# Performance work log

Measured on AMD Instinct MI355X. Metric: run time of the kernel, lower is better.

The kernel has to match this reference:

```python
import jax, jax.numpy as jnp
import numpy as np

H = 1024
S = 8192
B = 1  # module's broadcast in the weighted-sum step only supports B == 1


def setup_inputs() -> dict:
    key = jax.random.key(0)
    k1, k2, k3 = jax.random.split(key, 3)
    scale = 1.0 / np.sqrt(H)
    enc_out = jax.random.normal(k1, (B, S, H), dtype=jnp.float32)
    w1 = jax.random.normal(k2, (H, H), dtype=jnp.float32) * scale  # nn.Linear weight [out,in]
    w2 = jax.random.normal(k3, (H, H), dtype=jnp.float32) * scale
    return {"enc_out": enc_out, "w1": w1, "w2": w2}


def reference(enc_out, w1, w2):
    # attn_weights = tanh(w1(enc_out)) @ w2(enc_out)^T  -> [B, S, S]
    q = jnp.tanh(jnp.einsum('bsh,oh->bso', enc_out, w1))
    k = jnp.einsum('bsh,oh->bso', enc_out, w2)
    scores = jnp.einsum('bih,bjh->bij', q, k)          # [B, S, S]
    attn = jax.nn.softmax(scores, axis=1)               # softmax over dim=1 (rows)
    # torch: sum over dim=1 of attn[B,S,S,1] * enc_out broadcast as [1,B,S,H].
    # For B==1 this equals enc_out[0,j,h] * sum_i attn[0,i,j]; avoid the
    # [B,S,S,H] intermediate the eager torch code materializes.
    col_sum = jnp.sum(attn, axis=1)                     # [B, S]
    context = col_sum[..., None] * enc_out              # [B, S, H]
    return context, attn
```

## Files before the change

### kernel.cpp

```cpp
#include <hip/hip_runtime.h>
#include <hip/hip_bf16.h>
#include <math.h>


typedef _Float16 half_t;
typedef _Float16 half8 __attribute__((ext_vector_type(8)));
typedef _Float16 half4 __attribute__((ext_vector_type(4)));
typedef float f32x4 __attribute__((ext_vector_type(4)));

#define S_DIM 8192
#define H_DIM 1024

__device__ __forceinline__ void gload16(const void* g, void* l) {
  __builtin_amdgcn_global_load_lds(
      (const __attribute__((address_space(1))) void*)g,
      (__attribute__((address_space(3))) void*)l, 16, 0, 0);
}

__global__ void __launch_bounds__(256) k_cvt(const float* __restrict__ src,
                                             half_t* __restrict__ dst) {
  long g = (long)blockIdx.x * 256 + threadIdx.x;
  f32x4 x = ((const f32x4*)src)[g];
  half4 h;
#pragma unroll
  for (int e = 0; e < 4; ++e) h[e] = (half_t)x[e];
  ((half4*)dst)[g] = h;
}

#define GEMM_MAINLOOP(APTR, BPTR)                                              \
  __shared__ half_t As[8192];                                                  \
  __shared__ half_t Bs[8192];                                                  \
  const int tid = threadIdx.x;                                                 \
  const int lane = tid & 63;                                                   \
  const int quad = lane >> 4;                                                  \
  const int l15 = lane & 15;                                                   \
  const int wave = tid >> 6;                                                   \
  const int wm = wave & 1;                                                     \
  const int wn = wave >> 1;                                                    \
  int aoff[4], boff[4], loff[4];                                               \
  _Pragma("unroll") for (int t = 0; t < 4; ++t) {                              \
    int f8 = t * 256 + tid;                                                    \
    int u = f8 >> 7;                                                           \
    int m = f8 & 127;                                                          \
    aoff[t] = (bm * 128 + m) * H_DIM + u * 8;                                  \
    boff[t] = (bn * 128 + m) * H_DIM + u * 8;                                  \
    loff[t] = f8 * 8;                                                          \
  }                                                                            \
  f32x4 acc[4][4];                                                             \
  _Pragma("unroll") for (int r = 0; r < 4; ++r)                                \
      _Pragma("unroll") for (int c = 0; c < 4; ++c)                            \
          acc[r][c] = (f32x4){0.f, 0.f, 0.f, 0.f};                             \
  for (int k0 = 0; k0 < H_DIM; k0 += 64) {                                     \
    _Pragma("unroll") for (int t = 0; t < 4; ++t)                              \
        gload16(APTR + aoff[t] + k0, &As[loff[t]]);                            \
    _Pragma("unroll") for (int t = 0; t < 4; ++t)                              \
        gload16(BPTR + boff[t] + k0, &Bs[loff[t]]);                            \
    __syncthreads();                                                           \
    _Pragma("unroll") for (int ki = 0; ki < 2; ++ki) {                         \
      const int u = ki * 4 + quad;                                             \
      half8 af[4], bf[4];                                                      \
      _Pragma("unroll") for (int r = 0; r < 4; ++r)                            \
          af[r] = *(const half8*)&As[(u * 128 + wm * 64 + r * 16 + l15) * 8];  \
      _Pragma("unroll") for (int c = 0; c < 4; ++c)                            \
          bf[c] = *(const half8*)&Bs[(u * 128 + wn * 64 + c * 16 + l15) * 8];  \
      _Pragma("unroll") for (int r = 0; r < 4; ++r)                            \
          _Pragma("unroll") for (int c = 0; c < 4; ++c)                        \
              acc[r][c] = __builtin_amdgcn_mfma_f32_16x16x32_f16(              \
                  af[r], bf[c], acc[r][c], 0, 0, 0);                           \
    }                                                                          \
    __syncthreads();                                                           \
  }

__global__ void __launch_bounds__(256) k_gemm_qk(const half_t* __restrict__ A,
                                                 const half_t* __restrict__ B,
                                                 half_t* __restrict__ Qh,
                                                 half_t* __restrict__ Kh) {
  const int bm = blockIdx.y;
  const int bn = blockIdx.x;
  GEMM_MAINLOOP(A, B)
  const int colbase = bn * 128 + wn * 64;
  const int rowb = bm * 128 + wm * 64;
#pragma unroll
  for (int r = 0; r < 4; ++r) {
#pragma unroll
    for (int c = 0; c < 4; ++c) {
      int col = colbase + c * 16 + l15;
      int row = rowb + r * 16 + quad * 4;
#pragma unroll
      for (int v = 0; v < 4; ++v) {
        float x = acc[r][c][v];
        if (col < 1024) {
          Qh[(long)(row + v) * 1024 + col] = (half_t)tanhf(x);
        } else {
          Kh[(long)(row + v) * 1024 + (col - 1024)] = (half_t)x;
        }
      }
    }
  }
}

template <bool FUSE_STATS>
__global__ void __launch_bounds__(256) k_gemm_scores(const half_t* __restrict__ A,
                                                     const half_t* __restrict__ B,
                                                     float* __restrict__ out,
                                                     float* __restrict__ Pm,
                                                     float* __restrict__ Ps) {
  const int lin = blockIdx.x;
  const int patch = lin >> 6;
  const int local = lin & 63;
  const int bm = (patch >> 3) * 8 + (local >> 3);
  const int bn = (patch & 7) * 8 + (local & 7);
  GEMM_MAINLOOP(A, B)
  const int colbase = bn * 128 + wn * 64;
  const int rowb = bm * 128 + wm * 64;
#pragma unroll
  for (int r = 0; r < 4; ++r) {
#pragma unroll
    for (int c = 0; c < 4; ++c) {
      int col = colbase + c * 16 + l15;
      int row = rowb + r * 16 + quad * 4;
#pragma unroll
      for (int v = 0; v < 4; ++v) {
        out[(long)(row + v) * S_DIM + col] = acc[r][c][v];
      }
    }
  }
  if (FUSE_STATS) {
    float cmax[4], csum[4];
#pragma unroll
    for (int c = 0; c < 4; ++c) {
      float m = acc[0][c][0];
#pragma unroll
      for (int r = 0; r < 4; ++r)
#pragma unroll
        for (int v = 0; v < 4; ++v) m = fmaxf(m, acc[r][c][v]);
      m = fmaxf(m, __shfl_xor(m, 16, 64));
      m = fmaxf(m, __shfl_xor(m, 32, 64));
      cmax[c] = m;
      float s = 0.f;
#pragma unroll
      for (int r = 0; r < 4; ++r)
#pragma unroll
        for (int v = 0; v < 4; ++v) s += __expf(acc[r][c][v] - m);
      s += __shfl_xor(s, 16, 64);
      s += __shfl_xor(s, 32, 64);
      csum[c] = s;
    }
    float* sred = (float*)As;
    if (quad == 0) {
#pragma unroll
      for (int c = 0; c < 4; ++c) {
        int idx = ((((wm * 2 + wn) * 4 + c) * 16 + l15) * 2);
        sred[idx] = cmax[c];
        sred[idx + 1] = csum[c];
      }
    }
    __syncthreads();
    if (wm == 0 && quad == 0) {
#pragma unroll
      for (int c = 0; c < 4; ++c) {
        int i0 = ((((0 * 2 + wn) * 4 + c) * 16 + l15) * 2);
        int i1 = ((((1 * 2 + wn) * 4 + c) * 16 + l15) * 2);
        float m0 = sred[i0], s0 = sred[i0 + 1];
        float m1 = sred[i1], s1 = sred[i1 + 1];
        float M = fmaxf(m0, m1);
        float Ssum = s0 * __expf(m0 - M) + s1 * __expf(m1 - M);
        int col = colbase + c * 16 + l15;
        Pm[(long)bm * S_DIM + col] = M;
        Ps[(long)bm * S_DIM + col] = Ssum;
      }
    }
  }
}

__global__ void __launch_bounds__(256) k_colstats(const float* __restrict__ P,
                                                  float* __restrict__ Pm,
                                                  float* __restrict__ Ps) {
  const int c = threadIdx.x & 63;
  const int rg = threadIdx.x >> 6;
  const int j = blockIdx.x * 64 + c;
  const int seg = blockIdx.y;
  float m = -3.0e38f, s = 0.f;
  for (int t = 0; t < 256; ++t) {
    int i = seg * 1024 + t * 4 + rg;
    float x = P[(long)i * S_DIM + j];
    float mn = fmaxf(m, x);
    s = s * __expf(m - mn) + __expf(x - mn);
    m = mn;
  }
  __shared__ float sm[4][64];
  __shared__ float ss[4][64];
  sm[rg][c] = m;
  ss[rg][c] = s;
  __syncthreads();
  if (threadIdx.x < 64) {
    float mm = sm[0][c];
#pragma unroll
    for (int r = 1; r < 4; ++r) mm = fmaxf(mm, sm[r][c]);
    float sum = 0.f;
#pragma unroll
    for (int r = 0; r < 4; ++r) sum += ss[r][c] * __expf(sm[r][c] - mm);
    Pm[seg * S_DIM + j] = mm;
    Ps[seg * S_DIM + j] = sum;
  }
}

__global__ void __launch_bounds__(256) k_combine(const float* __restrict__ Pm,
                                                 const float* __restrict__ Ps,
                                                 float* __restrict__ Mcol,
                                                 float* __restrict__ Rcol,
                                                 int nseg) {
  int j = blockIdx.x * 256 + threadIdx.x;
  float m = Pm[j];
  for (int r = 1; r < nseg; ++r) m = fmaxf(m, Pm[(long)r * S_DIM + j]);
  float s = 0.f;
  for (int r = 0; r < nseg; ++r)
    s += Ps[(long)r * S_DIM + j] * __expf(Pm[(long)r * S_DIM + j] - m);
  Mcol[j] = m;
  Rcol[j] = 1.0f / s;
}

__global__ void __launch_bounds__(256) k_norm(float* __restrict__ P,
                                              const float* __restrict__ Mcol,
                                              const float* __restrict__ Rcol,
                                              const f32x4* __restrict__ enc,
                                              f32x4* __restrict__ ctx) {
  long b = blockIdx.x;
  if (b >= 65536) {
    long g = (b - 65536) * 256 + threadIdx.x;
    ctx[g] = enc[g];
    return;
  }
  long gid = b * 256 + threadIdx.x;
  int j4 = (int)(gid & 2047);
  f32x4 x = ((const f32x4*)P)[gid];
  f32x4 a = ((const f32x4*)Mcol)[j4];
  f32x4 r = ((const f32x4*)Rcol)[j4];
  f32x4 o;
#pragma unroll
  for (int e = 0; e < 4; ++e) o[e] = __expf(x[e] - a[e]) * r[e];
  ((f32x4*)P)[gid] = o;
}

extern "C" void kernel_launch(void* const* d_in, const int* in_sizes, int n_in,
                              void* d_out, int out_size, void* d_ws, size_t ws_size,
                              hipStream_t stream) {
  const float* enc = (const float*)d_in[0];
  const float* w1 = (const float*)d_in[1];
  const float* w2 = (const float*)d_in[2];

  float* out = (float*)d_out;
  float* ctx = out;
  float* attn = out + 8388608;

  half_t* Qh = (half_t*)ctx;
  half_t* Kh = Qh + 8388608;
  half_t* enc_h = (half_t*)attn;
  half_t* w_h = (half_t*)((char*)attn + 16777216);

  const bool fuse = ws_size >= (size_t)(64 + 64 + 2) * S_DIM * 4;
  const int nseg = fuse ? 64 : 8;
  char* ws = (char*)d_ws;
  float* Pm = (float*)ws;
  float* Ps = (float*)(ws + (size_t)nseg * S_DIM * 4);
  float* Mcol = (float*)(ws + (size_t)2 * nseg * S_DIM * 4);
  float* Rcol = Mcol + S_DIM;

  k_cvt<<<8192, 256, 0, stream>>>(enc, enc_h);
  k_cvt<<<1024, 256, 0, stream>>>(w1, w_h);
  k_cvt<<<1024, 256, 0, stream>>>(w2, w_h + 1048576);

  k_gemm_qk<<<dim3(16, 64), 256, 0, stream>>>(enc_h, w_h, Qh, Kh);

  if (fuse) {
    k_gemm_scores<true><<<4096, 256, 0, stream>>>(Qh, Kh, attn, Pm, Ps);
  } else {
    k_gemm_scores<false><<<4096, 256, 0, stream>>>(Qh, Kh, attn, Pm, Ps);
    k_colstats<<<dim3(128, 8), 256, 0, stream>>>(attn, Pm, Ps);
  }
  k_combine<<<32, 256, 0, stream>>>(Pm, Ps, Mcol, Rcol, nseg);

  k_norm<<<73728, 256, 0, stream>>>(attn, Mcol, Rcol, (const f32x4*)enc,
                                    (f32x4*)ctx);
}
```

Measured before the change: 766.8 us.

## Use 256x256 GEMM tiles with a 4-stage async LDS pipeline

```diff
diff --git a/kernel.cpp b/kernel.cpp
--- a/kernel.cpp
+++ b/kernel.cpp
@@ -16,6 +16,8 @@
       (const __attribute__((address_space(1))) void*)g,
       (__attribute__((address_space(3))) void*)l, 16, 0, 0);
 }
+
+#define WAITVM(N) asm volatile("s_waitcnt vmcnt(" #N ")" ::: "memory")
 
 __global__ void __launch_bounds__(256) k_cvt(const float* __restrict__ src,
                                              half_t* __restrict__ dst) {
@@ -27,97 +29,112 @@
   ((half4*)dst)[g] = h;
 }
 
-#define GEMM_MAINLOOP(APTR, BPTR)                                              \
-  __shared__ half_t As[8192];                                                  \
-  __shared__ half_t Bs[8192];                                                  \
+#define GEMM_MAINLOOP_256(APTR, BPTR)                                          \
+  __shared__ __align__(16) half_t As[4][8192];                                 \
+  __shared__ __align__(16) half_t Bs[4][8192];                                 \
   const int tid = threadIdx.x;                                                 \
   const int lane = tid & 63;                                                   \
   const int quad = lane >> 4;                                                  \
   const int l15 = lane & 15;                                                   \
   const int wave = tid >> 6;                                                   \
-  const int wm = wave & 1;                                                     \
-  const int wn = wave >> 1;                                                    \
-  int aoff[4], boff[4], loff[4];                                               \
-  _Pragma("unroll") for (int t = 0; t < 4; ++t) {                              \
-    int f8 = t * 256 + tid;                                                    \
-    int u = f8 >> 7;                                                           \
-    int m = f8 & 127;                                                          \
-    aoff[t] = (bm * 128 + m) * H_DIM + u * 8;                                  \
-    boff[t] = (bn * 128 + m) * H_DIM + u * 8;                                  \
+  const int wm = wave >> 2;                                          \
+  const int wn = wave & 3;                                           \
+  int aoff[2], boff[2], loff[2];                                               \
+  _Pragma("unroll") for (int t = 0; t < 2; ++t) {                              \
+    int f8 = t * 512 + tid;                                       \
+    int u = f8 >> 8;                                                 \
+    int m = f8 & 255;                                                          \
+    aoff[t] = (bm * 256 + m) * H_DIM + u * 8;                                  \
+    boff[t] = (bn * 256 + m) * H_DIM + u * 8;                                  \
     loff[t] = f8 * 8;                                                          \
   }                                                                            \
-  f32x4 acc[4][4];                                                             \
-  _Pragma("unroll") for (int r = 0; r < 4; ++r)                                \
+  f32x4 acc[8][4];                                                             \
+  _Pragma("unroll") for (int r = 0; r < 8; ++r)                                \
       _Pragma("unroll") for (int c = 0; c < 4; ++c)                            \
           acc[r][c] = (f32x4){0.f, 0.f, 0.f, 0.f};                             \
-  for (int k0 = 0; k0 < H_DIM; k0 += 64) {                                     \
-    _Pragma("unroll") for (int t = 0; t < 4; ++t)                              \
-        gload16(APTR + aoff[t] + k0, &As[loff[t]]);                            \
-    _Pragma("unroll") for (int t = 0; t < 4; ++t)                              \
-        gload16(BPTR + boff[t] + k0, &Bs[loff[t]]);                            \
-    __syncthreads();                                                           \
-    _Pragma("unroll") for (int ki = 0; ki < 2; ++ki) {                         \
-      const int u = ki * 4 + quad;                                             \
-      half8 af[4], bf[4];                                                      \
-      _Pragma("unroll") for (int r = 0; r < 4; ++r)                            \
-          af[r] = *(const half8*)&As[(u * 128 + wm * 64 + r * 16 + l15) * 8];  \
-      _Pragma("unroll") for (int c = 0; c < 4; ++c)                            \
-          bf[c] = *(const half8*)&Bs[(u * 128 + wn * 64 + c * 16 + l15) * 8];  \
-      _Pragma("unroll") for (int r = 0; r < 4; ++r)                            \
-          _Pragma("unroll") for (int c = 0; c < 4; ++c)                        \
-              acc[r][c] = __builtin_amdgcn_mfma_f32_16x16x32_f16(              \
-                  af[r], bf[c], acc[r][c], 0, 0, 0);                           \
+               \
+  _Pragma("unroll") for (int pc = 0; pc < 3; ++pc)                             \
+      _Pragma("unroll") for (int t = 0; t < 2; ++t) {                          \
+    gload16(APTR + aoff[t] + pc * 32, &As[pc][loff[t]]);                       \
+    gload16(BPTR + boff[t] + pc * 32, &Bs[pc][loff[t]]);                       \
+  }                                                                            \
+  const int abase = (quad * 256 + wm * 128 + l15) * 8;                         \
+  const int bbase = (quad * 256 + wn * 64 + l15) * 8;                          \
+  _Pragma("unroll 1") for (int ch = 0; ch < 32; ++ch) {                        \
+    const int buf = ch & 3;                                                    \
+    if (ch <= 29) { WAITVM(8); }           \
+    else if (ch == 30) { WAITVM(4); }                                          \
+    else { WAITVM(0); }                                                        \
+    __builtin_amdgcn_s_barrier();                                              \
+    asm volatile("" ::: "memory");        \
+    if (ch + 3 < 32) {  \
+      const int nb = (ch + 3) & 3;                                             \
+      _Pragma("unroll") for (int t = 0; t < 2; ++t) {                          \
+        gload16(APTR + aoff[t] + (ch + 3) * 32, &As[nb][loff[t]]);             \
+        gload16(BPTR + boff[t] + (ch + 3) * 32, &Bs[nb][loff[t]]);             \
+      }                                                                        \
     }                                                                          \
-    __syncthreads();                                                           \
-  }
-
-__global__ void __launch_bounds__(256) k_gemm_qk(const half_t* __restrict__ A,
-                                                 const half_t* __restrict__ B,
-                                                 half_t* __restrict__ Qh,
-                                                 half_t* __restrict__ Kh) {
+    half8 af[8], bf[4];                                                        \
+    _Pragma("unroll") for (int r = 0; r < 8; ++r)                              \
+        af[r] = *(const half8*)&As[buf][abase + r * 128];                      \
+    _Pragma("unroll") for (int c = 0; c < 4; ++c)                              \
+        bf[c] = *(const half8*)&Bs[buf][bbase + c * 128];                      \
+    __builtin_amdgcn_s_setprio(1);                                             \
+    _Pragma("unroll") for (int r = 0; r < 8; ++r)                              \
+        _Pragma("unroll") for (int c = 0; c < 4; ++c)                          \
+            acc[r][c] = __builtin_amdgcn_mfma_f32_16x16x32_f16(                \
+                af[r], bf[c], acc[r][c], 0, 0, 0);                             \
+    __builtin_amdgcn_s_setprio(0);                                             \
+  }
+
+__global__ void __launch_bounds__(512, 2) k_gemm_qk(const half_t* __restrict__ A,
+                                                    const half_t* __restrict__ B,
+                                                    half_t* __restrict__ Qh,
+                                                    half_t* __restrict__ Kh) {
   const int bm = blockIdx.y;
   const int bn = blockIdx.x;
-  GEMM_MAINLOOP(A, B)
-  const int colbase = bn * 128 + wn * 64;
-  const int rowb = bm * 128 + wm * 64;
-#pragma unroll
-  for (int r = 0; r < 4; ++r) {
+  GEMM_MAINLOOP_256(A, B)
+  const int colb = bn * 256 + wn * 64;
+  const int rowb = bm * 256 + wm * 128;
+  const bool isQ = (bn < 4);
+#pragma unroll
+  for (int r = 0; r < 8; ++r) {
 #pragma unroll
     for (int c = 0; c < 4; ++c) {
-      int col = colbase + c * 16 + l15;
+      int col = colb + c * 16 + l15;
       int row = rowb + r * 16 + quad * 4;
-#pragma unroll
-      for (int v = 0; v < 4; ++v) {
-        float x = acc[r][c][v];
-        if (col < 1024) {
-          Qh[(long)(row + v) * 1024 + col] = (half_t)tanhf(x);
-        } else {
-          Kh[(long)(row + v) * 1024 + (col - 1024)] = (half_t)x;
-        }
+      if (isQ) {
+#pragma unroll
+        for (int v = 0; v < 4; ++v)
+          Qh[(long)(row + v) * 1024 + col] = (half_t)tanhf(acc[r][c][v]);
+      } else {
+#pragma unroll
+        for (int v = 0; v < 4; ++v)
+          Kh[(long)(row + v) * 1024 + (col - 1024)] = (half_t)acc[r][c][v];
       }
     }
   }
 }
 
 template <bool FUSE_STATS>
-__global__ void __launch_bounds__(256) k_gemm_scores(const half_t* __restrict__ A,
-                                                     const half_t* __restrict__ B,
-                                                     float* __restrict__ out,
-                                                     float* __restrict__ Pm,
-                                                     float* __restrict__ Ps) {
+__global__ void __launch_bounds__(512, 2) k_gemm_scores(const half_t* __restrict__ A,
+                                                        const half_t* __restrict__ B,
+                                                        float* __restrict__ out,
+                                                        float* __restrict__ Pm,
+                                                        float* __restrict__ Ps) {
   const int lin = blockIdx.x;
   const int patch = lin >> 6;
   const int local = lin & 63;
-  const int bm = (patch >> 3) * 8 + (local >> 3);
-  const int bn = (patch & 7) * 8 + (local & 7);
-  GEMM_MAINLOOP(A, B)
-  const int colbase = bn * 128 + wn * 64;
-  const int rowb = bm * 128 + wm * 64;
-#pragma unroll
-  for (int r = 0; r < 4; ++r) {
+  const int bm = (patch >> 2) * 8 + (local >> 3);
+  const int bn = (patch & 3) * 8 + (local & 7);
+  GEMM_MAINLOOP_256(A, B)
+  const int colb = bn * 256 + wn * 64;
+  const int rowb = bm * 256 + wm * 128;
+#pragma unroll
+  for (int r = 0; r < 8; ++r) {
 #pragma unroll
     for (int c = 0; c < 4; ++c) {
-      int col = colbase + c * 16 + l15;
+      int col = colb + c * 16 + l15;
       int row = rowb + r * 16 + quad * 4;
 #pragma unroll
       for (int v = 0; v < 4; ++v) {
@@ -131,7 +148,7 @@
     for (int c = 0; c < 4; ++c) {
       float m = acc[0][c][0];
 #pragma unroll
-      for (int r = 0; r < 4; ++r)
+      for (int r = 0; r < 8; ++r)
 #pragma unroll
         for (int v = 0; v < 4; ++v) m = fmaxf(m, acc[r][c][v]);
       m = fmaxf(m, __shfl_xor(m, 16, 64));
@@ -139,7 +156,7 @@
       cmax[c] = m;
       float s = 0.f;
 #pragma unroll
-      for (int r = 0; r < 4; ++r)
+      for (int r = 0; r < 8; ++r)
 #pragma unroll
         for (int v = 0; v < 4; ++v) s += __expf(acc[r][c][v] - m);
       s += __shfl_xor(s, 16, 64);
@@ -150,7 +167,7 @@
     if (quad == 0) {
 #pragma unroll
       for (int c = 0; c < 4; ++c) {
-        int idx = ((((wm * 2 + wn) * 4 + c) * 16 + l15) * 2);
+        int idx = (((wm * 4 + wn) * 4 + c) * 16 + l15) * 2;
         sred[idx] = cmax[c];
         sred[idx + 1] = csum[c];
       }
@@ -159,13 +176,13 @@
     if (wm == 0 && quad == 0) {
 #pragma unroll
       for (int c = 0; c < 4; ++c) {
-        int i0 = ((((0 * 2 + wn) * 4 + c) * 16 + l15) * 2);
-        int i1 = ((((1 * 2 + wn) * 4 + c) * 16 + l15) * 2);
+        int i0 = (((0 * 4 + wn) * 4 + c) * 16 + l15) * 2;
+        int i1 = (((1 * 4 + wn) * 4 + c) * 16 + l15) * 2;
         float m0 = sred[i0], s0 = sred[i0 + 1];
         float m1 = sred[i1], s1 = sred[i1 + 1];
         float M = fmaxf(m0, m1);
         float Ssum = s0 * __expf(m0 - M) + s1 * __expf(m1 - M);
-        int col = colbase + c * 16 + l15;
+        int col = colb + c * 16 + l15;
         Pm[(long)bm * S_DIM + col] = M;
         Ps[(long)bm * S_DIM + col] = Ssum;
       }
@@ -258,8 +275,8 @@
   half_t* enc_h = (half_t*)attn;
   half_t* w_h = (half_t*)((char*)attn + 16777216);
 
-  const bool fuse = ws_size >= (size_t)(64 + 64 + 2) * S_DIM * 4;
-  const int nseg = fuse ? 64 : 8;
+  const bool fuse = ws_size >= (size_t)(32 + 32 + 2) * S_DIM * 4;
+  const int nseg = fuse ? 32 : 8;
   char* ws = (char*)d_ws;
   float* Pm = (float*)ws;
   float* Ps = (float*)(ws + (size_t)nseg * S_DIM * 4);
@@ -270,12 +287,12 @@
   k_cvt<<<1024, 256, 0, stream>>>(w1, w_h);
   k_cvt<<<1024, 256, 0, stream>>>(w2, w_h + 1048576);
 
-  k_gemm_qk<<<dim3(16, 64), 256, 0, stream>>>(enc_h, w_h, Qh, Kh);
+  k_gemm_qk<<<dim3(8, 32), 512, 0, stream>>>(enc_h, w_h, Qh, Kh);
 
   if (fuse) {
-    k_gemm_scores<true><<<4096, 256, 0, stream>>>(Qh, Kh, attn, Pm, Ps);
+    k_gemm_scores<true><<<1024, 512, 0, stream>>>(Qh, Kh, attn, Pm, Ps);
   } else {
-    k_gemm_scores<false><<<4096, 256, 0, stream>>>(Qh, Kh, attn, Pm, Ps);
+    k_gemm_scores<false><<<1024, 512, 0, stream>>>(Qh, Kh, attn, Pm, Ps);
     k_colstats<<<dim3(128, 8), 256, 0, stream>>>(attn, Pm, Ps);
   }
   k_combine<<<32, 256, 0, stream>>>(Pm, Ps, Mcol, Rcol, nseg);
```

Result: slower. 785.7 us (+2.5%).
